# Optimization experiments

Measured on AMD Instinct MI355X. Metric: run time of the kernel, lower is better.

Reference implementation:

```python
import jax, jax.numpy as jnp
import numpy as np
import math

JULIA_ITERS = 64
ESCAPE_RADIUS = 2.0


def _julia_escape_times(seq_len, c_real, c_imag):
    # Positions mapped to the real segment [-2, 2]; iterate z <- z^2 + c,
    # record (first iteration index where |z| > R) / ITERS, else 1.0.
    x = jnp.linspace(-2.0, 2.0, seq_len)
    zr0 = x
    zi0 = jnp.zeros_like(x)
    escaped0 = jnp.zeros(seq_len, dtype=bool)
    et0 = jnp.ones(seq_len, dtype=x.dtype)
    r2 = ESCAPE_RADIUS * ESCAPE_RADIUS

    def step(carry, it):
        zr, zi, escaped, et = carry
        nzr = zr * zr - zi * zi + c_real
        nzi = 2.0 * zr * zi + c_imag
        # torch breaks out of the loop once escaped -> freeze z afterwards
        zr = jnp.where(escaped, zr, nzr)
        zi = jnp.where(escaped, zi, nzi)
        mag2 = zr * zr + zi * zi
        newly = jnp.logical_and(~escaped, mag2 > r2)
        et = jnp.where(newly, it.astype(et.dtype) / JULIA_ITERS, et)
        escaped = jnp.logical_or(escaped, newly)
        return (zr, zi, escaped, et), None

    (_, _, _, et), _ = jax.lax.scan(step, (zr0, zi0, escaped0, et0), jnp.arange(JULIA_ITERS))
    return et


def setup_inputs() -> dict:
    key = jax.random.key(0)
    kq, kk, kv = jax.random.split(key, 3)
    B, S, D = 4, 8192, 64
    return {
        "query": jax.random.normal(kq, (B, S, D), dtype=jnp.float32),
        "key": jax.random.normal(kk, (B, S, D), dtype=jnp.float32),
        "value": jax.random.normal(kv, (B, S, D), dtype=jnp.float32),
        "julia_c_real": jnp.float32(-0.7),
        "julia_c_imag": jnp.float32(0.27),
        "escape_scale": jnp.float32(1.0),
    }


def reference(query, key, value, julia_c_real, julia_c_imag, escape_scale):
    B, S, D = key.shape
    et = _julia_escape_times(S, julia_c_real, julia_c_imag)            # [S]
    julia_weights = jnp.exp(et * escape_scale)                          # [S]
    bias = jnp.log(julia_weights + 1e-8)                                # [S]
    scores = jnp.einsum("bqd,bkd->bqk", query, key) / math.sqrt(D)     # [B,S,S]
    scores = scores + bias[None, None, :]
    attn = jax.nn.softmax(scores, axis=-1)
    out = jnp.einsum("bqk,bkd->bqd", attn, value)                       # [B,S,D]
    return out  # squeeze(1) is a no-op for S > 1
```

## Files before the change

### kernel.cpp

```cpp
#include <hip/hip_runtime.h>
#include <math.h>

#define S_LEN 8192
#define DHEAD 64
#define NBATCH 4
#define BQ 64
#define BK 32
#define KIT 64

typedef unsigned short u16;
typedef unsigned int u32;
typedef __attribute__((ext_vector_type(8))) short short8;
typedef __attribute__((ext_vector_type(4))) short short4v;
typedef __attribute__((ext_vector_type(4))) float f32x4;

union U16x8 { int4 i4; short8 s8; };
union U16x4 { int2 i2; short4v s4; };

#if __has_builtin(__builtin_amdgcn_exp2f)
#define EXP2(x) __builtin_amdgcn_exp2f(x)
#else
#define EXP2(x) exp2f(x)
#endif

__device__ __forceinline__ u16 f2b(float f) {
    u32 u = __float_as_uint(f);
    u32 r = (u + 0x7fffu + ((u >> 16) & 1u)) >> 16;
    return (u16)r;
}

__device__ __forceinline__ u32 pack2(float a, float b) {
    u32 ua = __float_as_uint(a) + 0x8000u;
    u32 ub = __float_as_uint(b) + 0x8000u;
    return __builtin_amdgcn_perm(ub, ua, 0x07060302u);
}

__device__ __forceinline__ void load_lds16(const u16* g, u16* l) {
    __builtin_amdgcn_global_load_lds(
        (const __attribute__((address_space(1))) u32*)g,
        (__attribute__((address_space(3))) u32*)l, 16, 0, 0);
}

__global__ void julia_bias_kernel(const float* crp, const float* cip,
                                  const float* scp, float* bias2) {
#pragma clang fp contract(off)
    int i = blockIdx.x * 256 + threadIdx.x;
    if (i >= S_LEN) return;
    double cr = (double)crp[0], ci = (double)cip[0], sc = (double)scp[0];
    double step = 4.0 / (double)(S_LEN - 1);
    double x = (i == S_LEN - 1) ? 2.0 : (-2.0 + step * (double)i);
    double zr = x, zi = 0.0, et = 1.0;
    bool esc = false;
    for (int it = 0; it < 64; ++it) {
        double nzr = zr * zr - zi * zi + cr;
        double nzi = 2.0 * zr * zi + ci;
        if (!esc) { zr = nzr; zi = nzi; }
        double m2 = zr * zr + zi * zi;
        if (!esc && m2 > 4.0) { et = (double)it / 64.0; esc = true; }
    }
    double bias = log(exp(et * sc) + 1e-8);
    bias2[i] = (float)(bias * 1.4426950408889634 - 20.0);
}

__global__ void prep_kernel(const float* __restrict__ K, const float* __restrict__ V,
                            u16* __restrict__ Kb, u16* __restrict__ Vt) {
    int bid = blockIdx.x, tid = threadIdx.x;
    if (bid < 512) {
        __shared__ float tile[64][65];
        int b = bid >> 7;
        int s0 = (bid & 127) * 64;
        int c4 = (tid & 15) * 4;
        int rr = tid >> 4;
#pragma unroll
        for (int p = 0; p < 4; ++p) {
            int row = p * 16 + rr;
            float4 v = *(const float4*)(V + ((size_t)(b * S_LEN + s0 + row)) * DHEAD + c4);
            tile[row][c4 + 0] = v.x; tile[row][c4 + 1] = v.y;
            tile[row][c4 + 2] = v.z; tile[row][c4 + 3] = v.w;
        }
        __syncthreads();
#pragma unroll
        for (int p = 0; p < 4; ++p) {
            int d = p * 16 + rr;
            u32 lo = (u32)f2b(tile[c4 + 0][d]) | ((u32)f2b(tile[c4 + 1][d]) << 16);
            u32 hi = (u32)f2b(tile[c4 + 2][d]) | ((u32)f2b(tile[c4 + 3][d]) << 16);
            int c4p = c4 ^ (d & 4);
            *(uint2*)(Vt + ((size_t)(b * DHEAD + d)) * S_LEN + s0 + c4p) = make_uint2(lo, hi);
        }
    } else {
        size_t base = ((size_t)(bid - 512) * 256 + tid) * 16;
#pragma unroll
        for (int j = 0; j < 4; ++j) {
            float4 v = *(const float4*)(K + base + j * 4);
            u32 lo = (u32)f2b(v.x) | ((u32)f2b(v.y) << 16);
            u32 hi = (u32)f2b(v.z) | ((u32)f2b(v.w) << 16);
            *(uint2*)(Kb + base + j * 4) = make_uint2(lo, hi);
        }
    }
}

__global__ __launch_bounds__(512, 4)
void flash_kernel(const float* __restrict__ Q, const u16* __restrict__ Kb,
                  const u16* __restrict__ Vt, const float* __restrict__ bias2,
                  float* __restrict__ Out) {
    __shared__ __align__(16) char smem[65536];
    u16* K_lds = (u16*)smem;
    u16* V_lds = (u16*)(smem + 32768);

    const int tid = threadIdx.x;
    const int w = tid >> 6, l = tid & 63, low = l & 15, h = l >> 4;
    const int kq = w & 3, qs = w >> 2;

    const int bid = blockIdx.x;
    const int batch = (bid & 7) >> 1;
    const int qtile = ((bid >> 3) << 1) | (bid & 1);
    const int q0w = qtile * BQ + qs * 32;

    const float qscale = 0.18033688011112042f;
    short8 qfrag[2][2];
#pragma unroll
    for (int qf = 0; qf < 2; ++qf) {
        const float* qrow = Q + ((size_t)(batch * S_LEN + q0w + qf * 16 + low)) * DHEAD + h * 8;
#pragma unroll
        for (int ds = 0; ds < 2; ++ds) {
            f32x4 a = *(const f32x4*)(qrow + ds * 32);
            f32x4 b = *(const f32x4*)(qrow + ds * 32 + 4);
            U16x8 u;
#pragma unroll
            for (int j = 0; j < 4; ++j) {
                u.s8[j]     = (short)f2b(a[j] * qscale);
                u.s8[4 + j] = (short)f2b(b[j] * qscale);
            }
            qfrag[qf][ds] = u.s8;
        }
    }

    const u16 *kp0, *kp1, *vp0, *vp1;
    {
        int g0 = tid, g1 = tid + 512;
        int gq0 = g0 >> 8, tl0 = g0 & 255, gq1 = g1 >> 8, tl1 = g1 & 255;
        int gr0 = tl0 >> 3, gp0 = tl0 & 7;
        int gr1 = tl1 >> 3, gp1 = tl1 & 7;
        kp0 = Kb + ((size_t)(batch * S_LEN + gq0 * 2048 + gr0)) * 64 + (gp0 ^ (gr0 & 7)) * 8;
        kp1 = Kb + ((size_t)(batch * S_LEN + gq1 * 2048 + gr1)) * 64 + (gp1 ^ (gr1 & 7)) * 8;
        int d0 = tl0 >> 2, vg0 = tl0 & 3;
        int d1 = tl1 >> 2, vg1 = tl1 & 3;
        vp0 = Vt + ((size_t)(batch * DHEAD + d0)) * S_LEN + gq0 * 2048 + (vg0 ^ (d0 & 3)) * 8;
        vp1 = Vt + ((size_t)(batch * DHEAD + d1)) * S_LEN + gq1 * 2048 + (vg1 ^ (d1 & 3)) * 8;
    }
    const int dst0 = tid * 8, dst1 = tid * 8 + 4096;

    load_lds16(kp0, K_lds + dst0);
    load_lds16(kp1, K_lds + dst1);
    load_lds16(vp0, V_lds + dst0);
    load_lds16(vp1, V_lds + dst1);
    kp0 += BK * DHEAD; kp1 += BK * DHEAD; vp0 += BK; vp1 += BK;

    int koff[2][2], voff[4][2];
#pragma unroll
    for (int kt = 0; kt < 2; ++kt)
#pragma unroll
        for (int ds = 0; ds < 2; ++ds)
            koff[kt][ds] = kq * 2048 + (kt * 16 + low) * 64 + (((ds * 4 + h) ^ (low & 7)) * 8);
#pragma unroll
    for (int dt = 0; dt < 4; ++dt) {
        const int d = dt * 16 + low;
#pragma unroll
        for (int kt = 0; kt < 2; ++kt)
            voff[dt][kt] = kq * 2048 + d * 32 + (((kt * 2 + (h >> 1)) ^ (d & 3)) * 8) +
                           ((((h & 1) ^ (d >> 2)) & 1) * 4);
    }

    f32x4 o0[4], o1[4];
#pragma unroll
    for (int dt = 0; dt < 4; ++dt) { o0[dt] = (f32x4){0,0,0,0}; o1[dt] = (f32x4){0,0,0,0}; }
    float lsum0 = 0.f, lsum1 = 0.f;
    const float* b2p = bias2 + kq * 2048 + h * 4;

    for (int ki = 0; ki < KIT; ++ki) {
        __syncthreads();
        const int pb = ki & 1;
        if (ki != KIT - 1) {
            const int db = (pb ^ 1) * 8192;
            load_lds16(kp0, K_lds + db + dst0);
            load_lds16(kp1, K_lds + db + dst1);
            load_lds16(vp0, V_lds + db + dst0);
            load_lds16(vp1, V_lds + db + dst1);
            kp0 += BK * DHEAD; kp1 += BK * DHEAD; vp0 += BK; vp1 += BK;
        }
        const u16* kb_l = K_lds + pb * 8192;
        const u16* vb_l = V_lds + pb * 8192;

        f32x4 bv0 = *(const f32x4*)(b2p);
        f32x4 bv1 = *(const f32x4*)(b2p + 16);
        b2p += BK;

        f32x4 st0[2], st1[2];
#pragma unroll
        for (int kt = 0; kt < 2; ++kt) {
            f32x4 a0 = kt ? bv1 : bv0;
            f32x4 a1 = a0;
#pragma unroll
            for (int ds = 0; ds < 2; ++ds) {
                U16x8 u;
                u.i4 = *(const int4*)&kb_l[koff[kt][ds]];
                a0 = __builtin_amdgcn_mfma_f32_16x16x32_bf16(u.s8, qfrag[0][ds], a0, 0, 0, 0);
                a1 = __builtin_amdgcn_mfma_f32_16x16x32_bf16(u.s8, qfrag[1][ds], a1, 0, 0, 0);
            }
            st0[kt] = a0; st1[kt] = a1;
        }

        short4v pf0[2], pf1[2];
#pragma unroll
        for (int kt = 0; kt < 2; ++kt) {
            float p0 = EXP2(st0[kt][0]), p1 = EXP2(st0[kt][1]);
            float p2 = EXP2(st0[kt][2]), p3 = EXP2(st0[kt][3]);
            lsum0 += (p0 + p1) + (p2 + p3);
            U16x4 u; u.i2 = make_int2((int)pack2(p0, p1), (int)pack2(p2, p3));
            pf0[kt] = u.s4;
            float q0 = EXP2(st1[kt][0]), q1 = EXP2(st1[kt][1]);
            float q2 = EXP2(st1[kt][2]), q3 = EXP2(st1[kt][3]);
            lsum1 += (q0 + q1) + (q2 + q3);
            U16x4 v; v.i2 = make_int2((int)pack2(q0, q1), (int)pack2(q2, q3));
            pf1[kt] = v.s4;
        }

#pragma unroll
        for (int dt = 0; dt < 4; ++dt) {
#pragma unroll
            for (int kt = 0; kt < 2; ++kt) {
                U16x4 v;
                v.i2 = *(const int2*)&vb_l[voff[dt][kt]];
                o0[dt] = __builtin_amdgcn_mfma_f32_16x16x16bf16_1k(v.s4, pf0[kt], o0[dt], 0, 0, 0);
                o1[dt] = __builtin_amdgcn_mfma_f32_16x16x16bf16_1k(v.s4, pf1[kt], o1[dt], 0, 0, 0);
            }
        }
    }

    lsum0 += __shfl_xor(lsum0, 16, 64); lsum0 += __shfl_xor(lsum0, 32, 64);
    lsum1 += __shfl_xor(lsum1, 16, 64); lsum1 += __shfl_xor(lsum1, 32, 64);

    float* MO = (float*)smem;
    float* ML = (float*)(smem + 17408);
    const int row0 = qs * 32 + low;
    const int row1 = row0 + 16;
#pragma unroll 1
    for (int src = 1; src < 4; ++src) {
        __syncthreads();
        if (kq == src) {
#pragma unroll
            for (int dt = 0; dt < 4; ++dt) {
                *(f32x4*)&MO[row0 * 68 + dt * 16 + h * 4] = o0[dt];
                *(f32x4*)&MO[row1 * 68 + dt * 16 + h * 4] = o1[dt];
            }
            if (h == 0) { ML[row0] = lsum0; ML[row1] = lsum1; }
        }
        __syncthreads();
        if (kq == 0) {
#pragma unroll
            for (int dt = 0; dt < 4; ++dt) {
                f32x4 a = *(const f32x4*)&MO[row0 * 68 + dt * 16 + h * 4];
                f32x4 b = *(const f32x4*)&MO[row1 * 68 + dt * 16 + h * 4];
#pragma unroll
                for (int j = 0; j < 4; ++j) { o0[dt][j] += a[j]; o1[dt][j] += b[j]; }
            }
            lsum0 += ML[row0]; lsum1 += ML[row1];
        }
    }

    if (kq == 0) {
        const float inv0 = 1.f / lsum0, inv1 = 1.f / lsum1;
        float* orow0 = Out + ((size_t)(batch * S_LEN + qtile * BQ + row0)) * DHEAD;
        float* orow1 = Out + ((size_t)(batch * S_LEN + qtile * BQ + row1)) * DHEAD;
#pragma unroll
        for (int dt = 0; dt < 4; ++dt) {
            f32x4 r0, r1;
#pragma unroll
            for (int j = 0; j < 4; ++j) { r0[j] = o0[dt][j] * inv0; r1[j] = o1[dt][j] * inv1; }
            *(f32x4*)(orow0 + dt * 16 + h * 4) = r0;
            *(f32x4*)(orow1 + dt * 16 + h * 4) = r1;
        }
    }
}

extern "C" void kernel_launch(void* const* d_in, const int* in_sizes, int n_in,
                              void* d_out, int out_size, void* d_ws, size_t ws_size,
                              hipStream_t stream) {
    const float* Q  = (const float*)d_in[0];
    const float* K  = (const float*)d_in[1];
    const float* V  = (const float*)d_in[2];
    const float* cr = (const float*)d_in[3];
    const float* ci = (const float*)d_in[4];
    const float* sc = (const float*)d_in[5];
    float* out = (float*)d_out;

    char* ws = (char*)d_ws;
    float* bias2 = (float*)ws;
    u16*   Kb    = (u16*)(ws + 32768);
    u16*   Vt    = (u16*)(ws + 32768 + (size_t)NBATCH * S_LEN * DHEAD * 2);

    julia_bias_kernel<<<dim3(S_LEN / 256), dim3(256), 0, stream>>>(cr, ci, sc, bias2);
    prep_kernel<<<dim3(1024), dim3(256), 0, stream>>>(K, V, Kb, Vt);
    flash_kernel<<<dim3(512), dim3(512), 0, stream>>>(Q, Kb, Vt, bias2, out);
}
```

Before: 181.4 us.

## Double query tile per block, use 16x16x32 MFMA for PV, merge bias into prep

Each block now handles 128 query rows, with each wave owning 64 rows, so every K/V fragment read from LDS feeds four query fragments instead of two. The PV product switches from 16x16x16 to 16x16x32 bf16 MFMA. To supply full 8-element P fragments, the K rows are permuted and the K/V LDS swizzles are redone. The Julia bias computation is folded into the prep kernel to save a launch, and bias loads are prefetched one iteration ahead. The cost is more accumulator registers (launch bounds drop to 2 blocks per CU) and only 256 blocks, half the CU-level parallelism.

Measured after the change: 190.4 us. 5.0% more time.

```diff
diff --git a/kernel.cpp b/kernel.cpp
--- a/kernel.cpp
+++ b/kernel.cpp
@@ -4,18 +4,16 @@
 #define S_LEN 8192
 #define DHEAD 64
 #define NBATCH 4
-#define BQ 64
+#define BQ 128
 #define BK 32
 #define KIT 64
 
 typedef unsigned short u16;
 typedef unsigned int u32;
 typedef __attribute__((ext_vector_type(8))) short short8;
-typedef __attribute__((ext_vector_type(4))) short short4v;
 typedef __attribute__((ext_vector_type(4))) float f32x4;
 
-union U16x8 { int4 i4; short8 s8; };
-union U16x4 { int2 i2; short4v s4; };
+union U16x8 { int4 i4; short8 s8; u32 w[4]; };
 
 #if __has_builtin(__builtin_amdgcn_exp2f)
 #define EXP2(x) __builtin_amdgcn_exp2f(x)
@@ -41,29 +39,13 @@
         (__attribute__((address_space(3))) u32*)l, 16, 0, 0);
 }
 
-__global__ void julia_bias_kernel(const float* crp, const float* cip,
-                                  const float* scp, float* bias2) {
-#pragma clang fp contract(off)
-    int i = blockIdx.x * 256 + threadIdx.x;
-    if (i >= S_LEN) return;
-    double cr = (double)crp[0], ci = (double)cip[0], sc = (double)scp[0];
-    double step = 4.0 / (double)(S_LEN - 1);
-    double x = (i == S_LEN - 1) ? 2.0 : (-2.0 + step * (double)i);
-    double zr = x, zi = 0.0, et = 1.0;
-    bool esc = false;
-    for (int it = 0; it < 64; ++it) {
-        double nzr = zr * zr - zi * zi + cr;
-        double nzi = 2.0 * zr * zi + ci;
-        if (!esc) { zr = nzr; zi = nzi; }
-        double m2 = zr * zr + zi * zi;
-        if (!esc && m2 > 4.0) { et = (double)it / 64.0; esc = true; }
-    }
-    double bias = log(exp(et * sc) + 1e-8);
-    bias2[i] = (float)(bias * 1.4426950408889634 - 20.0);
-}
+__device__ __forceinline__ int swzK(int r) { return (r & 3) | ((r >> 1) & 4); }
+__device__ __forceinline__ int swzV(int d) { return (d & 3) ^ ((d >> 2) & 3); }
 
 __global__ void prep_kernel(const float* __restrict__ K, const float* __restrict__ V,
-                            u16* __restrict__ Kb, u16* __restrict__ Vt) {
+                            const float* crp, const float* cip, const float* scp,
+                            u16* __restrict__ Kb, u16* __restrict__ Vt,
+                            float* __restrict__ bias2) {
     int bid = blockIdx.x, tid = threadIdx.x;
     if (bid < 512) {
         __shared__ float tile[64][65];
@@ -84,10 +66,9 @@
             int d = p * 16 + rr;
             u32 lo = (u32)f2b(tile[c4 + 0][d]) | ((u32)f2b(tile[c4 + 1][d]) << 16);
             u32 hi = (u32)f2b(tile[c4 + 2][d]) | ((u32)f2b(tile[c4 + 3][d]) << 16);
-            int c4p = c4 ^ (d & 4);
-            *(uint2*)(Vt + ((size_t)(b * DHEAD + d)) * S_LEN + s0 + c4p) = make_uint2(lo, hi);
-        }
-    } else {
+            *(uint2*)(Vt + ((size_t)(b * DHEAD + d)) * S_LEN + s0 + c4) = make_uint2(lo, hi);
+        }
+    } else if (bid < 1024) {
         size_t base = ((size_t)(bid - 512) * 256 + tid) * 16;
 #pragma unroll
         for (int j = 0; j < 4; ++j) {
@@ -96,10 +77,27 @@
             u32 hi = (u32)f2b(v.z) | ((u32)f2b(v.w) << 16);
             *(uint2*)(Kb + base + j * 4) = make_uint2(lo, hi);
         }
-    }
-}
-
-__global__ __launch_bounds__(512, 4)
+    } else {
+#pragma clang fp contract(off)
+        int i = (bid - 1024) * 256 + tid;
+        double cr = (double)crp[0], ci = (double)cip[0], sc = (double)scp[0];
+        double step = 4.0 / (double)(S_LEN - 1);
+        double x = (i == S_LEN - 1) ? 2.0 : (-2.0 + step * (double)i);
+        double zr = x, zi = 0.0, et = 1.0;
+        bool esc = false;
+        for (int it = 0; it < 64; ++it) {
+            double nzr = zr * zr - zi * zi + cr;
+            double nzi = 2.0 * zr * zi + ci;
+            if (!esc) { zr = nzr; zi = nzi; }
+            double m2 = zr * zr + zi * zi;
+            if (!esc && m2 > 4.0) { et = (double)it / 64.0; esc = true; }
+        }
+        double bias = log(exp(et * sc) + 1e-8);
+        bias2[i] = (float)(bias * 1.4426950408889634 - 20.0);
+    }
+}
+
+__global__ __launch_bounds__(512, 2)
 void flash_kernel(const float* __restrict__ Q, const u16* __restrict__ Kb,
                   const u16* __restrict__ Vt, const float* __restrict__ bias2,
                   float* __restrict__ Out) {
@@ -112,15 +110,15 @@
     const int kq = w & 3, qs = w >> 2;
 
     const int bid = blockIdx.x;
-    const int batch = (bid & 7) >> 1;
-    const int qtile = ((bid >> 3) << 1) | (bid & 1);
-    const int q0w = qtile * BQ + qs * 32;
+    const int batch = bid & 3;
+    const int qtile = bid >> 2;
+    const int q0 = qtile * BQ + qs * 64;
 
     const float qscale = 0.18033688011112042f;
-    short8 qfrag[2][2];
-#pragma unroll
-    for (int qf = 0; qf < 2; ++qf) {
-        const float* qrow = Q + ((size_t)(batch * S_LEN + q0w + qf * 16 + low)) * DHEAD + h * 8;
+    short8 qfrag[4][2];
+#pragma unroll
+    for (int qf = 0; qf < 4; ++qf) {
+        const float* qrow = Q + ((size_t)(batch * S_LEN + q0 + qf * 16 + low)) * DHEAD + h * 8;
 #pragma unroll
         for (int ds = 0; ds < 2; ++ds) {
             f32x4 a = *(const f32x4*)(qrow + ds * 32);
@@ -137,16 +135,14 @@
 
     const u16 *kp0, *kp1, *vp0, *vp1;
     {
-        int g0 = tid, g1 = tid + 512;
-        int gq0 = g0 >> 8, tl0 = g0 & 255, gq1 = g1 >> 8, tl1 = g1 & 255;
-        int gr0 = tl0 >> 3, gp0 = tl0 & 7;
-        int gr1 = tl1 >> 3, gp1 = tl1 & 7;
-        kp0 = Kb + ((size_t)(batch * S_LEN + gq0 * 2048 + gr0)) * 64 + (gp0 ^ (gr0 & 7)) * 8;
-        kp1 = Kb + ((size_t)(batch * S_LEN + gq1 * 2048 + gr1)) * 64 + (gp1 ^ (gr1 & 7)) * 8;
-        int d0 = tl0 >> 2, vg0 = tl0 & 3;
-        int d1 = tl1 >> 2, vg1 = tl1 & 3;
-        vp0 = Vt + ((size_t)(batch * DHEAD + d0)) * S_LEN + gq0 * 2048 + (vg0 ^ (d0 & 3)) * 8;
-        vp1 = Vt + ((size_t)(batch * DHEAD + d1)) * S_LEN + gq1 * 2048 + (vg1 ^ (d1 & 3)) * 8;
+        int kqs = tid >> 8, r = (tid >> 3) & 31, gph = tid & 7;
+        int gl = gph ^ swzK(r);
+        kp0 = Kb + ((size_t)(batch * S_LEN + kqs * 2048 + r)) * 64 + gl * 8;
+        kp1 = kp0 + (size_t)2 * 2048 * 64;
+        int dv = (tid >> 2) & 63, gphv = tid & 3;
+        int glv = gphv ^ swzV(dv);
+        vp0 = Vt + ((size_t)(batch * DHEAD + dv)) * S_LEN + kqs * 2048 + glv * 8;
+        vp1 = vp0 + 2 * 2048;
     }
     const int dst0 = tid * 8, dst1 = tid * 8 + 4096;
 
@@ -156,26 +152,31 @@
     load_lds16(vp1, V_lds + dst1);
     kp0 += BK * DHEAD; kp1 += BK * DHEAD; vp0 += BK; vp1 += BK;
 
-    int koff[2][2], voff[4][2];
-#pragma unroll
-    for (int kt = 0; kt < 2; ++kt)
+    int koff[2][2], voff[4];
+#pragma unroll
+    for (int kt = 0; kt < 2; ++kt) {
+        const int R = 8 * (low >> 2) + 4 * kt + (low & 3);
 #pragma unroll
         for (int ds = 0; ds < 2; ++ds)
-            koff[kt][ds] = kq * 2048 + (kt * 16 + low) * 64 + (((ds * 4 + h) ^ (low & 7)) * 8);
+            koff[kt][ds] = kq * 2048 + R * 64 + (((ds * 4 + h) ^ swzK(R)) * 8);
+    }
 #pragma unroll
     for (int dt = 0; dt < 4; ++dt) {
         const int d = dt * 16 + low;
-#pragma unroll
-        for (int kt = 0; kt < 2; ++kt)
-            voff[dt][kt] = kq * 2048 + d * 32 + (((kt * 2 + (h >> 1)) ^ (d & 3)) * 8) +
-                           ((((h & 1) ^ (d >> 2)) & 1) * 4);
-    }
-
-    f32x4 o0[4], o1[4];
-#pragma unroll
-    for (int dt = 0; dt < 4; ++dt) { o0[dt] = (f32x4){0,0,0,0}; o1[dt] = (f32x4){0,0,0,0}; }
-    float lsum0 = 0.f, lsum1 = 0.f;
-    const float* b2p = bias2 + kq * 2048 + h * 4;
+        voff[dt] = kq * 2048 + d * 32 + ((h ^ swzV(d)) * 8);
+    }
+
+    f32x4 o[4][4];
+#pragma unroll
+    for (int qf = 0; qf < 4; ++qf)
+#pragma unroll
+        for (int dt = 0; dt < 4; ++dt) o[qf][dt] = (f32x4){0, 0, 0, 0};
+    float lsum[4] = {0.f, 0.f, 0.f, 0.f};
+
+    const float* b2p = bias2 + kq * 2048 + h * 8;
+    f32x4 bv0 = *(const f32x4*)b2p;
+    f32x4 bv1 = *(const f32x4*)(b2p + 4);
+    b2p += BK;
 
     for (int ki = 0; ki < KIT; ++ki) {
         __syncthreads();
@@ -188,97 +189,102 @@
             load_lds16(vp1, V_lds + db + dst1);
             kp0 += BK * DHEAD; kp1 += BK * DHEAD; vp0 += BK; vp1 += BK;
         }
-        const u16* kb_l = K_lds + pb * 8192;
-        const u16* vb_l = V_lds + pb * 8192;
-
-        f32x4 bv0 = *(const f32x4*)(b2p);
-        f32x4 bv1 = *(const f32x4*)(b2p + 16);
+        f32x4 bvn0 = *(const f32x4*)b2p;
+        f32x4 bvn1 = *(const f32x4*)(b2p + 4);
         b2p += BK;
 
-        f32x4 st0[2], st1[2];
+        const u16* kb = K_lds + pb * 8192;
+        const u16* vb = V_lds + pb * 8192;
+
+        f32x4 st[4][2];
 #pragma unroll
         for (int kt = 0; kt < 2; ++kt) {
-            f32x4 a0 = kt ? bv1 : bv0;
-            f32x4 a1 = a0;
-#pragma unroll
-            for (int ds = 0; ds < 2; ++ds) {
-                U16x8 u;
-                u.i4 = *(const int4*)&kb_l[koff[kt][ds]];
-                a0 = __builtin_amdgcn_mfma_f32_16x16x32_bf16(u.s8, qfrag[0][ds], a0, 0, 0, 0);
-                a1 = __builtin_amdgcn_mfma_f32_16x16x32_bf16(u.s8, qfrag[1][ds], a1, 0, 0, 0);
-            }
-            st0[kt] = a0; st1[kt] = a1;
-        }
-
-        short4v pf0[2], pf1[2];
-#pragma unroll
-        for (int kt = 0; kt < 2; ++kt) {
-            float p0 = EXP2(st0[kt][0]), p1 = EXP2(st0[kt][1]);
-            float p2 = EXP2(st0[kt][2]), p3 = EXP2(st0[kt][3]);
-            lsum0 += (p0 + p1) + (p2 + p3);
-            U16x4 u; u.i2 = make_int2((int)pack2(p0, p1), (int)pack2(p2, p3));
-            pf0[kt] = u.s4;
-            float q0 = EXP2(st1[kt][0]), q1 = EXP2(st1[kt][1]);
-            float q2 = EXP2(st1[kt][2]), q3 = EXP2(st1[kt][3]);
-            lsum1 += (q0 + q1) + (q2 + q3);
-            U16x4 v; v.i2 = make_int2((int)pack2(q0, q1), (int)pack2(q2, q3));
-            pf1[kt] = v.s4;
+            U16x8 k0, k1;
+            k0.i4 = *(const int4*)&kb[koff[kt][0]];
+            k1.i4 = *(const int4*)&kb[koff[kt][1]];
+            const f32x4 binit = kt ? bv1 : bv0;
+#pragma unroll
+            for (int qf = 0; qf < 4; ++qf) {
+                f32x4 a = __builtin_amdgcn_mfma_f32_16x16x32_bf16(k0.s8, qfrag[qf][0], binit, 0, 0, 0);
+                a = __builtin_amdgcn_mfma_f32_16x16x32_bf16(k1.s8, qfrag[qf][1], a, 0, 0, 0);
+                st[qf][kt] = a;
+            }
+        }
+        bv0 = bvn0; bv1 = bvn1;
+
+        U16x8 pf[4];
+#pragma unroll
+        for (int qf = 0; qf < 4; ++qf) {
+#pragma unroll
+            for (int kt = 0; kt < 2; ++kt) {
+                float p0 = EXP2(st[qf][kt][0]), p1 = EXP2(st[qf][kt][1]);
+                float p2 = EXP2(st[qf][kt][2]), p3 = EXP2(st[qf][kt][3]);
+                lsum[qf] += (p0 + p1) + (p2 + p3);
+                pf[qf].w[kt * 2]     = pack2(p0, p1);
+                pf[qf].w[kt * 2 + 1] = pack2(p2, p3);
+            }
         }
 
 #pragma unroll
         for (int dt = 0; dt < 4; ++dt) {
-#pragma unroll
-            for (int kt = 0; kt < 2; ++kt) {
-                U16x4 v;
-                v.i2 = *(const int2*)&vb_l[voff[dt][kt]];
-                o0[dt] = __builtin_amdgcn_mfma_f32_16x16x16bf16_1k(v.s4, pf0[kt], o0[dt], 0, 0, 0);
-                o1[dt] = __builtin_amdgcn_mfma_f32_16x16x16bf16_1k(v.s4, pf1[kt], o1[dt], 0, 0, 0);
-            }
-        }
-    }
-
-    lsum0 += __shfl_xor(lsum0, 16, 64); lsum0 += __shfl_xor(lsum0, 32, 64);
-    lsum1 += __shfl_xor(lsum1, 16, 64); lsum1 += __shfl_xor(lsum1, 32, 64);
+            U16x8 vf;
+            vf.i4 = *(const int4*)&vb[voff[dt]];
+#pragma unroll
+            for (int qf = 0; qf < 4; ++qf)
+                o[qf][dt] = __builtin_amdgcn_mfma_f32_16x16x32_bf16(vf.s8, pf[qf].s8, o[qf][dt], 0, 0, 0);
+        }
+    }
+
+#pragma unroll
+    for (int qf = 0; qf < 4; ++qf) {
+        lsum[qf] += __shfl_xor(lsum[qf], 16, 64);
+        lsum[qf] += __shfl_xor(lsum[qf], 32, 64);
+    }
 
     float* MO = (float*)smem;
-    float* ML = (float*)(smem + 17408);
-    const int row0 = qs * 32 + low;
-    const int row1 = row0 + 16;
+    float* ML = (float*)(smem + 34816);
+    const int baserow = qs * 64 + low;
 #pragma unroll 1
     for (int src = 1; src < 4; ++src) {
         __syncthreads();
         if (kq == src) {
 #pragma unroll
-            for (int dt = 0; dt < 4; ++dt) {
-                *(f32x4*)&MO[row0 * 68 + dt * 16 + h * 4] = o0[dt];
-                *(f32x4*)&MO[row1 * 68 + dt * 16 + h * 4] = o1[dt];
-            }
-            if (h == 0) { ML[row0] = lsum0; ML[row1] = lsum1; }
+            for (int qf = 0; qf < 4; ++qf) {
+                const int row = baserow + qf * 16;
+#pragma unroll
+                for (int dt = 0; dt < 4; ++dt)
+                    *(f32x4*)&MO[row * 68 + dt * 16 + h * 4] = o[qf][dt];
+                if (h == 0) ML[row] = lsum[qf];
+            }
         }
         __syncthreads();
         if (kq == 0) {
 #pragma unroll
+            for (int qf = 0; qf < 4; ++qf) {
+                const int row = baserow + qf * 16;
+#pragma unroll
+                for (int dt = 0; dt < 4; ++dt) {
+                    f32x4 a = *(const f32x4*)&MO[row * 68 + dt * 16 + h * 4];
+#pragma unroll
+                    for (int j = 0; j < 4; ++j) o[qf][dt][j] += a[j];
+                }
+                lsum[qf] += ML[row];
+            }
+        }
+    }
+
+    if (kq == 0) {
+#pragma unroll
+        for (int qf = 0; qf < 4; ++qf) {
+            const float inv = 1.f / lsum[qf];
+            float* orow = Out + ((size_t)(batch * S_LEN + qtile * BQ + qs * 64 + qf * 16 + low)) * DHEAD;
+#pragma unroll
             for (int dt = 0; dt < 4; ++dt) {
-                f32x4 a = *(const f32x4*)&MO[row0 * 68 + dt * 16 + h * 4];
-                f32x4 b = *(const f32x4*)&MO[row1 * 68 + dt * 16 + h * 4];
-#pragma unroll
-                for (int j = 0; j < 4; ++j) { o0[dt][j] += a[j]; o1[dt][j] += b[j]; }
-            }
-            lsum0 += ML[row0]; lsum1 += ML[row1];
-        }
-    }
-
-    if (kq == 0) {
-        const float inv0 = 1.f / lsum0, inv1 = 1.f / lsum1;
-        float* orow0 = Out + ((size_t)(batch * S_LEN + qtile * BQ + row0)) * DHEAD;
-        float* orow1 = Out + ((size_t)(batch * S_LEN + qtile * BQ + row1)) * DHEAD;
-#pragma unroll
-        for (int dt = 0; dt < 4; ++dt) {
-            f32x4 r0, r1;
-#pragma unroll
-            for (int j = 0; j < 4; ++j) { r0[j] = o0[dt][j] * inv0; r1[j] = o1[dt][j] * inv1; }
-            *(f32x4*)(orow0 + dt * 16 + h * 4) = r0;
-            *(f32x4*)(orow1 + dt * 16 + h * 4) = r1;
+                f32x4 r;
+#pragma unroll
+                for (int j = 0; j < 4; ++j) r[j] = o[qf][dt][j] * inv;
+                *(f32x4*)(orow + dt * 16 + h * 4) = r;
+            }
         }
     }
 }
@@ -299,7 +305,6 @@
     u16*   Kb    = (u16*)(ws + 32768);
     u16*   Vt    = (u16*)(ws + 32768 + (size_t)NBATCH * S_LEN * DHEAD * 2);
 
-    julia_bias_kernel<<<dim3(S_LEN / 256), dim3(256), 0, stream>>>(cr, ci, sc, bias2);
-    prep_kernel<<<dim3(1024), dim3(256), 0, stream>>>(K, V, Kb, Vt);
-    flash_kernel<<<dim3(512), dim3(512), 0, stream>>>(Q, Kb, Vt, bias2, out);
-}
+    prep_kernel<<<dim3(1056), dim3(256), 0, stream>>>(K, V, cr, ci, sc, Kb, Vt, bias2);
+    flash_kernel<<<dim3(256), dim3(512), 0, stream>>>(Q, Kb, Vt, bias2, out);
+}
```
